# Kernel optimization log

Hardware: AMD Instinct MI355X
Metric: run time of the kernel (lower is better)

## Reference

```python
import jax, jax.numpy as jnp
import numpy as np
from jax import lax

B, C_IN, J, T = 32, 3, 64, 256
C_OUT = 64
S_LEN = 5           # spatial_length
T_LEN = 7           # temporal_length
T_PAD = (T_LEN - 1) // 2
EPS = 1e-5
SIG_IN = C_IN + 1   # +1 time channel from signatory.Augment(include_time=True)
SIG_CH = SIG_IN + SIG_IN**2 + SIG_IN**3  # signature_channels(depth=3) = 84


def sig3(pts):
    """Depth-3 path signature with basepoint=True. pts: [N, L, c] -> [N, c + c^2 + c^3]."""
    N, L, c = pts.shape
    # basepoint=True prepends the origin, so first increment is pts[:, 0]
    incs = jnp.concatenate([pts[:, :1], jnp.diff(pts, axis=1)], axis=1)  # [N, L, c]
    S1 = jnp.zeros((N, c), pts.dtype)
    S2 = jnp.zeros((N, c, c), pts.dtype)
    S3 = jnp.zeros((N, c, c, c), pts.dtype)

    def step(carry, d):  # Chen's identity: S <- S tensor exp(d)
        S1, S2, S3 = carry
        e2 = 0.5 * d[:, :, None] * d[:, None, :]               # d^2/2
        S3 = (S3
              + S2[:, :, :, None] * d[:, None, None, :]
              + S1[:, :, None, None] * e2[:, None, :, :]
              + d[:, :, None, None] * e2[:, None, :, :] / 3.0)  # d^3/6
        S2 = S2 + S1[:, :, None] * d[:, None, :] + e2
        S1 = S1 + d
        return (S1, S2, S3), None

    (S1, S2, S3), _ = lax.scan(step, (S1, S2, S3), jnp.swapaxes(incs, 0, 1))
    return jnp.concatenate([S1, S2.reshape(N, c * c), S3.reshape(N, c * c * c)], axis=1)


def signet(pts, W, b):
    """SigNet: time-augment, depth-3 signature, linear. pts: [N, L, C_IN]."""
    N, L, _ = pts.shape
    t = jnp.linspace(0.0, 1.0, L, dtype=pts.dtype)
    aug = jnp.concatenate([pts, jnp.broadcast_to(t[None, :, None], (N, L, 1))], axis=2)
    return sig3(aug) @ W.T + b


def bn(x, g, be, m, v):  # eval-mode BatchNorm2d, x [B,C,H,W]
    scale = (g / jnp.sqrt(v + EPS))[None, :, None, None]
    return (x - m[None, :, None, None]) * scale + be[None, :, None, None]


def setup_inputs() -> dict:
    key = jax.random.key(0)
    ks = jax.random.split(key, 12)
    d = {}
    d['x'] = jax.random.normal(ks[0], (B, C_IN, J, T), jnp.float32)
    d['path'] = jax.random.randint(ks[1], (J, S_LEN), 0, J, jnp.int32)
    d['W_ssig'] = jax.random.normal(ks[2], (C_OUT, SIG_CH), jnp.float32) * 0.05
    d['b_ssig'] = jnp.zeros((C_OUT,), jnp.float32)
    d['W_tsig'] = jax.random.normal(ks[3], (C_OUT, SIG_CH), jnp.float32) * 0.05
    d['b_tsig'] = jnp.zeros((C_OUT,), jnp.float32)
    d['W_raw'] = jax.random.normal(ks[4], (C_OUT, C_IN, 1, 3), jnp.float32) * 0.1
    d['b_raw'] = jnp.zeros((C_OUT,), jnp.float32)
    d['W_ps'] = jax.random.normal(ks[5], (C_OUT, 2 * C_OUT), jnp.float32) * 0.05
    d['b_ps'] = jnp.zeros((C_OUT,), jnp.float32)
    d['W_fu'] = jax.random.normal(ks[6], (C_OUT, 2 * C_OUT), jnp.float32) * 0.05
    d['b_fu'] = jnp.zeros((C_OUT,), jnp.float32)
    for tag in ('raw', 'ps', 'fu'):
        d['g_' + tag] = jnp.ones((C_OUT,), jnp.float32)
        d['be_' + tag] = jnp.zeros((C_OUT,), jnp.float32)
        d['m_' + tag] = jnp.zeros((C_OUT,), jnp.float32)
        d['v_' + tag] = jnp.ones((C_OUT,), jnp.float32)
    return d


def reference(x, path, W_ssig, b_ssig, W_tsig, b_tsig, W_raw, b_raw, W_ps, b_ps,
              W_fu, b_fu, g_raw, be_raw, m_raw, v_raw, g_ps, be_ps, m_ps, v_ps,
              g_fu, be_fu, m_fu, v_fu):
    Bx, C, Jx, Tx = x.shape
    # raw branch: Conv2d (1,3) pad (0,1) + BN + ReLU
    x_conv = lax.conv_general_dilated(x, W_raw, (1, 1), ((0, 0), (1, 1)),
                                      dimension_numbers=('NCHW', 'OIHW', 'NCHW'))
    x_conv = jax.nn.relu(bn(x_conv + b_raw[None, :, None, None], g_raw, be_raw, m_raw, v_raw))

    # spatial branch: gather joint paths -> [B*T*J, S_LEN, C]
    g = x[:, :, path, :]                                      # [B, C, J, S, T]
    sp = jnp.transpose(g, (0, 4, 2, 3, 1)).reshape(Bx * Tx * Jx, S_LEN, C)
    ss = signet(sp, W_ssig, b_ssig).reshape(Bx, Tx, Jx, C_OUT)
    ss = jnp.transpose(ss, (0, 3, 2, 1))                      # [B, C_OUT, J, T]

    # temporal branch: replicate-pad + unfold windows
    xp = jnp.pad(x, ((0, 0), (0, 0), (0, 0), (T_PAD, T_PAD)), mode='edge')
    tw = jnp.stack([xp[..., k:k + Tx] for k in range(T_LEN)], axis=2)  # [B, C, T_LEN, J, T]
    tw = tw.reshape(Bx, C, Jx, T_LEN, Tx)                     # faithful torch reshape (reinterprets memory)
    tp = jnp.transpose(tw, (0, 4, 2, 3, 1)).reshape(Bx * Tx * Jx, T_LEN, C)
    ts = signet(tp, W_tsig, b_tsig).reshape(Bx, Tx, Jx, C_OUT)
    ts = jnp.transpose(ts, (0, 3, 2, 1))                      # [B, C_OUT, J, T]

    # ps_fusion: 1x1 conv + BN + ReLU over concat(spatial, temporal)
    sig = jnp.concatenate([ss, ts], axis=1)                   # [B, 2*C_OUT, J, T]
    sig = jnp.einsum('oc,bcjt->bojt', W_ps, sig) + b_ps[None, :, None, None]
    sig = jax.nn.relu(bn(sig, g_ps, be_ps, m_ps, v_ps))

    # final fusion
    x_out = jnp.concatenate([x_conv, sig], axis=1)            # [B, 2*C_OUT, J, T]
    x_out = jnp.einsum('oc,bcjt->bojt', W_fu, x_out) + b_fu[None, :, None, None]
    x_out = jax.nn.relu(bn(x_out, g_fu, be_fu, m_fu, v_fu))
    return x_out
```

## Files before the change

### kernel.cpp

```cpp
#include <hip/hip_runtime.h>
#include <cstdint>

#define EPSF 1e-5f

typedef __attribute__((ext_vector_type(8))) short     bf16x8;
typedef __attribute__((ext_vector_type(4))) float     f32x4;
typedef __attribute__((ext_vector_type(4))) unsigned int uint32x4;
typedef __attribute__((ext_vector_type(2))) unsigned int uint32x2;

#define WS_B0 0
#define WS_BC 64
#define WS_BF 128

__device__ __forceinline__ unsigned short f2bf(float f) {
    union { float f; unsigned u; } v; v.f = f;
    unsigned r = v.u + 0x7fffu + ((v.u >> 16) & 1u);
    return (unsigned short)(r >> 16);
}

__device__ __forceinline__ unsigned cvtpk(float lo, float hi) {
    unsigned r;
    asm("v_cvt_pk_bf16_f32 %0, %1, %2" : "=v"(r) : "v"(lo), "v"(hi));
    return r;
}

__global__ __launch_bounds__(64) void stem_prep(
    const float* __restrict__ W_ssig, const float* __restrict__ b_ssig,
    const float* __restrict__ W_tsig, const float* __restrict__ b_tsig,
    const float* __restrict__ W_raw,  const float* __restrict__ b_raw,
    const float* __restrict__ W_ps,   const float* __restrict__ b_ps,
    const float* __restrict__ W_fu,   const float* __restrict__ b_fu,
    const float* __restrict__ g_raw, const float* __restrict__ be_raw,
    const float* __restrict__ m_raw, const float* __restrict__ v_raw,
    const float* __restrict__ g_ps,  const float* __restrict__ be_ps,
    const float* __restrict__ m_ps,  const float* __restrict__ v_ps,
    const float* __restrict__ g_fu,  const float* __restrict__ be_fu,
    const float* __restrict__ m_fu,  const float* __restrict__ v_fu,
    float* __restrict__ wsf, unsigned short* __restrict__ wsA1,
    unsigned short* __restrict__ wsA2, unsigned short* __restrict__ wsA3)
{
    const int l = threadIdx.x;
    const int f = blockIdx.x;
    if (f < 24) {
        const int h = f / 12, rem = f % 12, s = rem / 4, to = rem % 4;
        const int o = to*16 + (l & 15);
        const float sps = g_ps[o] / sqrtf(v_ps[o] + EPSF);
        const float* wp  = W_ps + o*128 + 64*h;
        const float* wsg = h ? W_tsig : W_ssig;
        for (int b = 0; b < 8; ++b) {
            const int k = s*32 + ((l >> 4) * 8) + b;
            float v = 0.f;
            if (k < 84) {
                float acc = 0.f;
                for (int c = 0; c < 64; ++c) acc = fmaf(wp[c], wsg[c*84 + k], acc);
                v = acc * sps;
            }
            wsA1[f*512 + l*8 + b] = f2bf(v);
        }
    } else if (f < 40) {
        const int q = f - 24, s = q / 4, to = q % 4;
        const int o = to*16 + (l & 15);
        const float sfu = g_fu[o] / sqrtf(v_fu[o] + EPSF);
        for (int b = 0; b < 8; ++b) {
            const int c = s*32 + ((l >> 4) * 8) + b;
            wsA2[q*512 + l*8 + b] = f2bf(W_fu[o*128 + c] * sfu);
        }
    } else if (f == 40) {
        const int o = l;
        const float sps = g_ps[o] / sqrtf(v_ps[o] + EPSF);
        float acc = b_ps[o] - m_ps[o];
        for (int c = 0; c < 64; ++c) {
            acc = fmaf(W_ps[o*128 + c],      b_ssig[c], acc);
            acc = fmaf(W_ps[o*128 + 64 + c], b_tsig[c], acc);
        }
        wsf[WS_B0 + o] = acc * sps + be_ps[o];
        const float sraw = g_raw[o] / sqrtf(v_raw[o] + EPSF);
        wsf[WS_BC + o] = (b_raw[o] - m_raw[o]) * sraw + be_raw[o];
        const float sfu = g_fu[o] / sqrtf(v_fu[o] + EPSF);
        wsf[WS_BF + o] = (b_fu[o] - m_fu[o]) * sfu + be_fu[o];
    } else {
        const int to = f - 41;
        const int o = to*16 + (l & 15);
        const float sraw = g_raw[o] / sqrtf(v_raw[o] + EPSF);
        for (int b = 0; b < 8; ++b) {
            const int k = ((l >> 4) * 8) + b;
            wsA3[to*512 + l*8 + b] = (k < 9) ? f2bf(W_raw[o*9 + k] * sraw) : (unsigned short)0;
        }
    }
}

__device__ __forceinline__ void sig_step(float* __restrict__ sig, const float d[4])
{
    float* S1 = sig; float* S2 = sig + 4; float* S3 = sig + 20;
    float dh[4], fv[4];
#pragma unroll
    for (int i = 0; i < 4; ++i) dh[i] = 0.5f * d[i];
#pragma unroll
    for (int i = 0; i < 4; ++i) fv[i] = fmaf(d[i], (1.f/3.f), S1[i]);
    float h[16];
#pragma unroll
    for (int i = 0; i < 4; ++i)
#pragma unroll
        for (int j = 0; j < 4; ++j) h[i*4+j] = fmaf(fv[i], dh[j], S2[i*4+j]);
#pragma unroll
    for (int i = 0; i < 4; ++i)
#pragma unroll
        for (int j = 0; j < 4; ++j) {
            const float hij = h[i*4+j];
#pragma unroll
            for (int k = 0; k < 4; ++k)
                S3[(i*4+j)*4+k] = fmaf(hij, d[k], S3[(i*4+j)*4+k]);
        }
    float q[4];
#pragma unroll
    for (int i = 0; i < 4; ++i) q[i] = S1[i] + dh[i];
#pragma unroll
    for (int i = 0; i < 4; ++i)
#pragma unroll
        for (int j = 0; j < 4; ++j) S2[i*4+j] = fmaf(q[i], d[j], S2[i*4+j]);
#pragma unroll
    for (int i = 0; i < 4; ++i) S1[i] += d[i];
}

__device__ __forceinline__ void sig_init(float* __restrict__ sig, float d0, float d1, float d2)
{
    const float dd[4] = { d0, d1, d2, 0.f };
#pragma unroll
    for (int i = 0; i < 4; ++i) sig[i] = dd[i];
#pragma unroll
    for (int i = 0; i < 4; ++i) {
        const float dh = 0.5f * dd[i];
#pragma unroll
        for (int j = 0; j < 4; ++j) sig[4 + i*4 + j] = dh * dd[j];
    }
#pragma unroll
    for (int i = 0; i < 4; ++i) {
        const float di3 = dd[i] * (1.f/3.f);
#pragma unroll
        for (int j = 0; j < 4; ++j)
#pragma unroll
            for (int k = 0; k < 4; ++k)
                sig[20 + (i*4+j)*4 + k] = di3 * sig[4 + j*4 + k];
    }
}

__global__ __launch_bounds__(64, 3) void stem_main(
    const float* __restrict__ x, const int* __restrict__ path,
    const float* __restrict__ wsf, const unsigned short* __restrict__ wsA1,
    const unsigned short* __restrict__ wsA2, const unsigned short* __restrict__ wsA3,
    float* __restrict__ out)
{
    __shared__ char sb[12 * 1024];
    const int l  = threadIdx.x;
    const int t  = blockIdx.x * 64 + l;
    const int j  = blockIdx.y;
    const int b  = blockIdx.z;
    const float* xb = x + (size_t)b * (3*64*256);

    const int lg = l >> 4;
    const int li = l & 15;
    char* const myw = sb + l*16;

    float ps_[5][3];
#pragma unroll
    for (int s = 0; s < 5; ++s) {
        const int jp = path[j*5 + s];
        ps_[s][0] = xb[(0*64 + jp)*256 + t];
        ps_[s][1] = xb[(1*64 + jp)*256 + t];
        ps_[s][2] = xb[(2*64 + jp)*256 + t];
    }
    float pt_[7][3];
#pragma unroll
    for (int k = 0; k < 7; ++k) {
        const int idx  = j*7 + k;
        const int jsrc = idx & 63;
        const int tl   = idx >> 6;
        const int ts   = min(max(t + tl - 3, 0), 255);
        pt_[k][0] = xb[(0*64 + jsrc)*256 + ts];
        pt_[k][1] = xb[(1*64 + jsrc)*256 + ts];
        pt_[k][2] = xb[(2*64 + jsrc)*256 + ts];
    }

    float sig[84];
    {
        sig_init(sig, ps_[0][0], ps_[0][1], ps_[0][2]);
#pragma unroll
        for (int s = 1; s < 5; ++s) {
            const float d[4] = { ps_[s][0]-ps_[s-1][0], ps_[s][1]-ps_[s-1][1],
                                 ps_[s][2]-ps_[s-1][2], 0.25f };
            sig_step(sig, d);
        }
    }
    {
        unsigned uu[48];
#pragma unroll
        for (int i = 0; i < 42; ++i) uu[i] = cvtpk(sig[2*i], sig[2*i+1]);
#pragma unroll
        for (int i = 42; i < 48; ++i) uu[i] = 0u;
#pragma unroll
        for (int v = 0; v < 12; ++v) {
            uint32x4 w = { uu[4*v], uu[4*v+1], uu[4*v+2], uu[4*v+3] };
            *(uint32x4*)(myw + v*1024) = w;
        }
    }
    __syncthreads();

    unsigned uuT[48];
    {
        sig_init(sig, pt_[0][0], pt_[0][1], pt_[0][2]);
#pragma unroll
        for (int k = 1; k < 7; ++k) {
            const float d[4] = { pt_[k][0]-pt_[k-1][0], pt_[k][1]-pt_[k-1][1],
                                 pt_[k][2]-pt_[k-1][2], (1.f/6.f) };
            sig_step(sig, d);
        }
#pragma unroll
        for (int i = 0; i < 42; ++i) uuT[i] = cvtpk(sig[2*i], sig[2*i+1]);
#pragma unroll
        for (int i = 42; i < 48; ++i) uuT[i] = 0u;
    }

    f32x4 acc[4][4];
#pragma unroll
    for (int to = 0; to < 4; ++to) {
        const f32x4 b0 = *(const f32x4*)(wsf + WS_B0 + to*16 + lg*4);
#pragma unroll
        for (int tt = 0; tt < 4; ++tt) acc[to][tt] = b0;
    }
    {
#pragma unroll
        for (int s = 0; s < 3; ++s) {
            bf16x8 A0 = *(const bf16x8*)(wsA1 + ((0*3+s)*4+0)*512 + l*8);
            bf16x8 A1 = *(const bf16x8*)(wsA1 + ((0*3+s)*4+1)*512 + l*8);
            bf16x8 A2 = *(const bf16x8*)(wsA1 + ((0*3+s)*4+2)*512 + l*8);
            bf16x8 A3 = *(const bf16x8*)(wsA1 + ((0*3+s)*4+3)*512 + l*8);
#pragma unroll
            for (int tt = 0; tt < 4; ++tt) {
                const bf16x8 B = *(const bf16x8*)(sb + (s*4+lg)*1024 + (tt*16+li)*16);
                acc[0][tt] = __builtin_amdgcn_mfma_f32_16x16x32_bf16(A0, B, acc[0][tt], 0, 0, 0);
                acc[1][tt] = __builtin_amdgcn_mfma_f32_16x16x32_bf16(A1, B, acc[1][tt], 0, 0, 0);
                acc[2][tt] = __builtin_amdgcn_mfma_f32_16x16x32_bf16(A2, B, acc[2][tt], 0, 0, 0);
                acc[3][tt] = __builtin_amdgcn_mfma_f32_16x16x32_bf16(A3, B, acc[3][tt], 0, 0, 0);
            }
        }
    }
    __syncthreads();

    {
#pragma unroll
        for (int v = 0; v < 12; ++v) {
            uint32x4 w = { uuT[4*v], uuT[4*v+1], uuT[4*v+2], uuT[4*v+3] };
            *(uint32x4*)(myw + v*1024) = w;
        }
    }
    __syncthreads();

    float xv[9];
#pragma unroll
    for (int ci = 0; ci < 3; ++ci) {
        const float* xr = xb + (ci*64 + j)*256;
        xv[ci*3+0] = (t >= 1)   ? xr[t-1] : 0.f;
        xv[ci*3+1] = xr[t];
        xv[ci*3+2] = (t <= 254) ? xr[t+1] : 0.f;
    }

    {
#pragma unroll
        for (int s = 0; s < 3; ++s) {
            bf16x8 A0 = *(const bf16x8*)(wsA1 + ((1*3+s)*4+0)*512 + l*8);
            bf16x8 A1 = *(const bf16x8*)(wsA1 + ((1*3+s)*4+1)*512 + l*8);
            bf16x8 A2 = *(const bf16x8*)(wsA1 + ((1*3+s)*4+2)*512 + l*8);
            bf16x8 A3 = *(const bf16x8*)(wsA1 + ((1*3+s)*4+3)*512 + l*8);
#pragma unroll
            for (int tt = 0; tt < 4; ++tt) {
                const bf16x8 B = *(const bf16x8*)(sb + (s*4+lg)*1024 + (tt*16+li)*16);
                acc[0][tt] = __builtin_amdgcn_mfma_f32_16x16x32_bf16(A0, B, acc[0][tt], 0, 0, 0);
                acc[1][tt] = __builtin_amdgcn_mfma_f32_16x16x32_bf16(A1, B, acc[1][tt], 0, 0, 0);
                acc[2][tt] = __builtin_amdgcn_mfma_f32_16x16x32_bf16(A2, B, acc[2][tt], 0, 0, 0);
                acc[3][tt] = __builtin_amdgcn_mfma_f32_16x16x32_bf16(A3, B, acc[3][tt], 0, 0, 0);
            }
        }
    }
    __syncthreads();

#pragma unroll
    for (int to = 0; to < 4; ++to) {
#pragma unroll
        for (int tt = 0; tt < 4; ++tt) {
            const unsigned w0 = cvtpk(fmaxf(acc[to][tt][0], 0.f), fmaxf(acc[to][tt][1], 0.f));
            const unsigned w1 = cvtpk(fmaxf(acc[to][tt][2], 0.f), fmaxf(acc[to][tt][3], 0.f));
            uint32x2 w = { w0, w1 };
            *(uint32x2*)(sb + (to*2+(lg>>1))*1024 + (tt*16+li)*16 + ((lg&1)<<3)) = w;
        }
    }
    {
        unsigned xu[16];
        xu[0] = cvtpk(xv[0], xv[1]); xu[1] = cvtpk(xv[2], xv[3]);
        xu[2] = cvtpk(xv[4], xv[5]); xu[3] = cvtpk(xv[6], xv[7]);
        xu[4] = cvtpk(xv[8], 0.f);
#pragma unroll
        for (int i = 5; i < 16; ++i) xu[i] = 0u;
#pragma unroll
        for (int v = 0; v < 4; ++v) {
            uint32x4 w = { xu[4*v], xu[4*v+1], xu[4*v+2], xu[4*v+3] };
            *(uint32x4*)(myw + (8+v)*1024) = w;
        }
    }
    __syncthreads();

#pragma unroll
    for (int to = 0; to < 4; ++to) {
        const f32x4 bc4 = *(const f32x4*)(wsf + WS_BC + to*16 + lg*4);
#pragma unroll
        for (int tt = 0; tt < 4; ++tt) acc[to][tt] = bc4;
    }
    {
        bf16x8 A0 = *(const bf16x8*)(wsA3 + 0*512 + l*8);
        bf16x8 A1 = *(const bf16x8*)(wsA3 + 1*512 + l*8);
        bf16x8 A2 = *(const bf16x8*)(wsA3 + 2*512 + l*8);
        bf16x8 A3 = *(const bf16x8*)(wsA3 + 3*512 + l*8);
#pragma unroll
        for (int tt = 0; tt < 4; ++tt) {
            const bf16x8 B = *(const bf16x8*)(sb + (8+lg)*1024 + (tt*16+li)*16);
            acc[0][tt] = __builtin_amdgcn_mfma_f32_16x16x32_bf16(A0, B, acc[0][tt], 0, 0, 0);
            acc[1][tt] = __builtin_amdgcn_mfma_f32_16x16x32_bf16(A1, B, acc[1][tt], 0, 0, 0);
            acc[2][tt] = __builtin_amdgcn_mfma_f32_16x16x32_bf16(A2, B, acc[2][tt], 0, 0, 0);
            acc[3][tt] = __builtin_amdgcn_mfma_f32_16x16x32_bf16(A3, B, acc[3][tt], 0, 0, 0);
        }
    }
    unsigned cu[32];
#pragma unroll
    for (int to = 0; to < 4; ++to)
#pragma unroll
        for (int tt = 0; tt < 4; ++tt) {
            cu[(to*4+tt)*2+0] = cvtpk(fmaxf(acc[to][tt][0], 0.f), fmaxf(acc[to][tt][1], 0.f));
            cu[(to*4+tt)*2+1] = cvtpk(fmaxf(acc[to][tt][2], 0.f), fmaxf(acc[to][tt][3], 0.f));
        }

#pragma unroll
    for (int to = 0; to < 4; ++to) {
        const f32x4 bf4 = *(const f32x4*)(wsf + WS_BF + to*16 + lg*4);
#pragma unroll
        for (int tt = 0; tt < 4; ++tt) acc[to][tt] = bf4;
    }
    {
#pragma unroll
        for (int s = 0; s < 2; ++s) {
            bf16x8 A0 = *(const bf16x8*)(wsA2 + ((s+2)*4+0)*512 + l*8);
            bf16x8 A1 = *(const bf16x8*)(wsA2 + ((s+2)*4+1)*512 + l*8);
            bf16x8 A2 = *(const bf16x8*)(wsA2 + ((s+2)*4+2)*512 + l*8);
            bf16x8 A3 = *(const bf16x8*)(wsA2 + ((s+2)*4+3)*512 + l*8);
#pragma unroll
            for (int tt = 0; tt < 4; ++tt) {
                const bf16x8 B = *(const bf16x8*)(sb + (s*4+lg)*1024 + (tt*16+li)*16);
                acc[0][tt] = __builtin_amdgcn_mfma_f32_16x16x32_bf16(A0, B, acc[0][tt], 0, 0, 0);
                acc[1][tt] = __builtin_amdgcn_mfma_f32_16x16x32_bf16(A1, B, acc[1][tt], 0, 0, 0);
                acc[2][tt] = __builtin_amdgcn_mfma_f32_16x16x32_bf16(A2, B, acc[2][tt], 0, 0, 0);
                acc[3][tt] = __builtin_amdgcn_mfma_f32_16x16x32_bf16(A3, B, acc[3][tt], 0, 0, 0);
            }
        }
    }
    __syncthreads();

#pragma unroll
    for (int to = 0; to < 4; ++to)
#pragma unroll
        for (int tt = 0; tt < 4; ++tt) {
            uint32x2 w = { cu[(to*4+tt)*2+0], cu[(to*4+tt)*2+1] };
            *(uint32x2*)(sb + (to*2+(lg>>1))*1024 + (tt*16+li)*16 + ((lg&1)<<3)) = w;
        }
    __syncthreads();

    {
#pragma unroll
        for (int s = 0; s < 2; ++s) {
            bf16x8 A0 = *(const bf16x8*)(wsA2 + (s*4+0)*512 + l*8);
            bf16x8 A1 = *(const bf16x8*)(wsA2 + (s*4+1)*512 + l*8);
            bf16x8 A2 = *(const bf16x8*)(wsA2 + (s*4+2)*512 + l*8);
            bf16x8 A3 = *(const bf16x8*)(wsA2 + (s*4+3)*512 + l*8);
#pragma unroll
            for (int tt = 0; tt < 4; ++tt) {
                const bf16x8 B = *(const bf16x8*)(sb + (s*4+lg)*1024 + (tt*16+li)*16);
                acc[0][tt] = __builtin_amdgcn_mfma_f32_16x16x32_bf16(A0, B, acc[0][tt], 0, 0, 0);
                acc[1][tt] = __builtin_amdgcn_mfma_f32_16x16x32_bf16(A1, B, acc[1][tt], 0, 0, 0);
                acc[2][tt] = __builtin_amdgcn_mfma_f32_16x16x32_bf16(A2, B, acc[2][tt], 0, 0, 0);
                acc[3][tt] = __builtin_amdgcn_mfma_f32_16x16x32_bf16(A3, B, acc[3][tt], 0, 0, 0);
            }
        }
    }

#pragma unroll
    for (int to = 0; to < 4; ++to) {
#pragma unroll
        for (int tt = 0; tt < 4; ++tt) {
            const int tg = blockIdx.x*64 + tt*16 + li;
#pragma unroll
            for (int r = 0; r < 4; ++r) {
                const int o = to*16 + lg*4 + r;
                out[(((size_t)b*64 + o)*64 + j)*256 + tg] = fmaxf(acc[to][tt][r], 0.f);
            }
        }
    }
}

extern "C" void kernel_launch(void* const* d_in, const int* in_sizes, int n_in,
                              void* d_out, int out_size, void* d_ws, size_t ws_size,
                              hipStream_t stream)
{
    const float* x      = (const float*)d_in[0];
    const int*   path   = (const int*)  d_in[1];
    const float* W_ssig = (const float*)d_in[2];
    const float* b_ssig = (const float*)d_in[3];
    const float* W_tsig = (const float*)d_in[4];
    const float* b_tsig = (const float*)d_in[5];
    const float* W_raw  = (const float*)d_in[6];
    const float* b_raw  = (const float*)d_in[7];
    const float* W_ps   = (const float*)d_in[8];
    const float* b_ps   = (const float*)d_in[9];
    const float* W_fu   = (const float*)d_in[10];
    const float* b_fu   = (const float*)d_in[11];
    const float* g_raw  = (const float*)d_in[12];
    const float* be_raw = (const float*)d_in[13];
    const float* m_raw  = (const float*)d_in[14];
    const float* v_raw  = (const float*)d_in[15];
    const float* g_ps   = (const float*)d_in[16];
    const float* be_ps  = (const float*)d_in[17];
    const float* m_ps   = (const float*)d_in[18];
    const float* v_ps   = (const float*)d_in[19];
    const float* g_fu   = (const float*)d_in[20];
    const float* be_fu  = (const float*)d_in[21];
    const float* m_fu   = (const float*)d_in[22];
    const float* v_fu   = (const float*)d_in[23];
    float* out = (float*)d_out;

    float*          wsf  = (float*)d_ws;
    unsigned short* wsA1 = (unsigned short*)((char*)d_ws + 4096);
    unsigned short* wsA2 = (unsigned short*)((char*)d_ws + 28672);
    unsigned short* wsA3 = (unsigned short*)((char*)d_ws + 45056);

    stem_prep<<<45, 64, 0, stream>>>(W_ssig, b_ssig, W_tsig, b_tsig, W_raw, b_raw,
                                     W_ps, b_ps, W_fu, b_fu,
                                     g_raw, be_raw, m_raw, v_raw,
                                     g_ps, be_ps, m_ps, v_ps,
                                     g_fu, be_fu, m_fu, v_fu, wsf, wsA1, wsA2, wsA3);

    dim3 grid(4, 64, 32);
    stem_main<<<grid, 64, 0, stream>>>(x, path, wsf, wsA1, wsA2, wsA3, out);
}
```

Measured before the change: 64.08 us.

## Compute path signatures in packed fp16 and switch MFMA to fp16

Replaces the fp32 scalar signature recurrence with packed-half arithmetic (v_pk_fma_f16 and op_sel broadcasts), so each instruction updates two signature terms and the state fits in 42 registers instead of 84. All MFMA operands and weights move from bf16 to fp16 to match, which removes the separate fp32-to-bf16 packing step. This roughly halves the VALU work and register pressure of the signature stage. The trade-off is reduced precision and range: the signature is accumulated in fp16 and conversions use round-toward-zero, which could overflow or lose accuracy on large inputs.

Result: faster. 60.57 us (-5.5%).

```diff
diff --git a/kernel.cpp b/kernel.cpp
--- a/kernel.cpp
+++ b/kernel.cpp
@@ -1,9 +1,10 @@
 #include <hip/hip_runtime.h>
+#include <hip/hip_fp16.h>
 #include <cstdint>
 
 #define EPSF 1e-5f
 
-typedef __attribute__((ext_vector_type(8))) short     bf16x8;
+typedef __attribute__((ext_vector_type(8))) _Float16  f16x8;
 typedef __attribute__((ext_vector_type(4))) float     f32x4;
 typedef __attribute__((ext_vector_type(4))) unsigned int uint32x4;
 typedef __attribute__((ext_vector_type(2))) unsigned int uint32x2;
@@ -12,17 +13,41 @@
 #define WS_BC 64
 #define WS_BF 128
 
-__device__ __forceinline__ unsigned short f2bf(float f) {
-    union { float f; unsigned u; } v; v.f = f;
-    unsigned r = v.u + 0x7fffu + ((v.u >> 16) & 1u);
-    return (unsigned short)(r >> 16);
-}
-
-__device__ __forceinline__ unsigned cvtpk(float lo, float hi) {
+__device__ __forceinline__ unsigned short f2h(float f) {
+    __half h = __float2half(f);
+    return *reinterpret_cast<unsigned short*>(&h);
+}
+
+__device__ __forceinline__ unsigned cvtpk_h(float lo, float hi) {
     unsigned r;
-    asm("v_cvt_pk_bf16_f32 %0, %1, %2" : "=v"(r) : "v"(lo), "v"(hi));
+    asm("v_cvt_pkrtz_f16_f32 %0, %1, %2" : "=v"(r) : "v"(lo), "v"(hi));
     return r;
 }
+
+__device__ __forceinline__ unsigned pkfma(unsigned a, unsigned b, unsigned c) {
+    unsigned d; asm("v_pk_fma_f16 %0, %1, %2, %3" : "=v"(d) : "v"(a), "v"(b), "v"(c)); return d;
+}
+__device__ __forceinline__ unsigned pkfma_lo(unsigned a, unsigned b, unsigned c) {
+    unsigned d; asm("v_pk_fma_f16 %0, %1, %2, %3 op_sel_hi:[0,1,1]" : "=v"(d) : "v"(a), "v"(b), "v"(c)); return d;
+}
+__device__ __forceinline__ unsigned pkfma_hi(unsigned a, unsigned b, unsigned c) {
+    unsigned d; asm("v_pk_fma_f16 %0, %1, %2, %3 op_sel:[1,0,0]" : "=v"(d) : "v"(a), "v"(b), "v"(c)); return d;
+}
+__device__ __forceinline__ unsigned pkmul(unsigned a, unsigned b) {
+    unsigned d; asm("v_pk_mul_f16 %0, %1, %2" : "=v"(d) : "v"(a), "v"(b)); return d;
+}
+__device__ __forceinline__ unsigned pkmul_lo(unsigned a, unsigned b) {
+    unsigned d; asm("v_pk_mul_f16 %0, %1, %2 op_sel_hi:[0,1]" : "=v"(d) : "v"(a), "v"(b)); return d;
+}
+__device__ __forceinline__ unsigned pkmul_hi(unsigned a, unsigned b) {
+    unsigned d; asm("v_pk_mul_f16 %0, %1, %2 op_sel:[1,0]" : "=v"(d) : "v"(a), "v"(b)); return d;
+}
+__device__ __forceinline__ unsigned pkadd(unsigned a, unsigned b) {
+    unsigned d; asm("v_pk_add_f16 %0, %1, %2" : "=v"(d) : "v"(a), "v"(b)); return d;
+}
+
+#define C_HALF2  0x38003800u
+#define C_THIRD2 0x35553555u
 
 __global__ __launch_bounds__(64) void stem_prep(
     const float* __restrict__ W_ssig, const float* __restrict__ b_ssig,
@@ -55,7 +80,7 @@
                 for (int c = 0; c < 64; ++c) acc = fmaf(wp[c], wsg[c*84 + k], acc);
                 v = acc * sps;
             }
-            wsA1[f*512 + l*8 + b] = f2bf(v);
+            wsA1[f*512 + l*8 + b] = f2h(v);
         }
     } else if (f < 40) {
         const int q = f - 24, s = q / 4, to = q % 4;
@@ -63,7 +88,7 @@
         const float sfu = g_fu[o] / sqrtf(v_fu[o] + EPSF);
         for (int b = 0; b < 8; ++b) {
             const int c = s*32 + ((l >> 4) * 8) + b;
-            wsA2[q*512 + l*8 + b] = f2bf(W_fu[o*128 + c] * sfu);
+            wsA2[q*512 + l*8 + b] = f2h(W_fu[o*128 + c] * sfu);
         }
     } else if (f == 40) {
         const int o = l;
@@ -84,63 +109,61 @@
         const float sraw = g_raw[o] / sqrtf(v_raw[o] + EPSF);
         for (int b = 0; b < 8; ++b) {
             const int k = ((l >> 4) * 8) + b;
-            wsA3[to*512 + l*8 + b] = (k < 9) ? f2bf(W_raw[o*9 + k] * sraw) : (unsigned short)0;
-        }
-    }
-}
-
-__device__ __forceinline__ void sig_step(float* __restrict__ sig, const float d[4])
+            wsA3[to*512 + l*8 + b] = (k < 9) ? f2h(W_raw[o*9 + k] * sraw) : (unsigned short)0;
+        }
+    }
+}
+
+__device__ __forceinline__ void sig_step_h(unsigned* __restrict__ S, unsigned d01, unsigned d23)
 {
-    float* S1 = sig; float* S2 = sig + 4; float* S3 = sig + 20;
-    float dh[4], fv[4];
-#pragma unroll
-    for (int i = 0; i < 4; ++i) dh[i] = 0.5f * d[i];
-#pragma unroll
-    for (int i = 0; i < 4; ++i) fv[i] = fmaf(d[i], (1.f/3.f), S1[i]);
-    float h[16];
-#pragma unroll
-    for (int i = 0; i < 4; ++i)
-#pragma unroll
-        for (int j = 0; j < 4; ++j) h[i*4+j] = fmaf(fv[i], dh[j], S2[i*4+j]);
-#pragma unroll
-    for (int i = 0; i < 4; ++i)
+    const unsigned dh0 = pkmul(C_HALF2, d01), dh1 = pkmul(C_HALF2, d23);
+    const unsigned fv0 = pkfma(d01, C_THIRD2, S[0]);
+    const unsigned fv1 = pkfma(d23, C_THIRD2, S[1]);
+    unsigned h[8];
+    h[0] = pkfma_lo(fv0, dh0, S[2]); h[1] = pkfma_lo(fv0, dh1, S[3]);
+    h[2] = pkfma_hi(fv0, dh0, S[4]); h[3] = pkfma_hi(fv0, dh1, S[5]);
+    h[4] = pkfma_lo(fv1, dh0, S[6]); h[5] = pkfma_lo(fv1, dh1, S[7]);
+    h[6] = pkfma_hi(fv1, dh0, S[8]); h[7] = pkfma_hi(fv1, dh1, S[9]);
+#pragma unroll
+    for (int i = 0; i < 4; ++i) {
 #pragma unroll
         for (int j = 0; j < 4; ++j) {
-            const float hij = h[i*4+j];
-#pragma unroll
-            for (int k = 0; k < 4; ++k)
-                S3[(i*4+j)*4+k] = fmaf(hij, d[k], S3[(i*4+j)*4+k]);
-        }
-    float q[4];
-#pragma unroll
-    for (int i = 0; i < 4; ++i) q[i] = S1[i] + dh[i];
-#pragma unroll
-    for (int i = 0; i < 4; ++i)
-#pragma unroll
-        for (int j = 0; j < 4; ++j) S2[i*4+j] = fmaf(q[i], d[j], S2[i*4+j]);
-#pragma unroll
-    for (int i = 0; i < 4; ++i) S1[i] += d[i];
-}
-
-__device__ __forceinline__ void sig_init(float* __restrict__ sig, float d0, float d1, float d2)
+            const int hr = i*2 + (j>>1);
+            const int base = 10 + (i*4+j)*2;
+            if (j & 1) { S[base]   = pkfma_hi(h[hr], d01, S[base]);
+                         S[base+1] = pkfma_hi(h[hr], d23, S[base+1]); }
+            else       { S[base]   = pkfma_lo(h[hr], d01, S[base]);
+                         S[base+1] = pkfma_lo(h[hr], d23, S[base+1]); }
+        }
+    }
+    const unsigned q0 = pkadd(S[0], dh0), q1 = pkadd(S[1], dh1);
+    S[2] = pkfma_lo(q0, d01, S[2]); S[3] = pkfma_lo(q0, d23, S[3]);
+    S[4] = pkfma_hi(q0, d01, S[4]); S[5] = pkfma_hi(q0, d23, S[5]);
+    S[6] = pkfma_lo(q1, d01, S[6]); S[7] = pkfma_lo(q1, d23, S[7]);
+    S[8] = pkfma_hi(q1, d01, S[8]); S[9] = pkfma_hi(q1, d23, S[9]);
+    S[0] = pkadd(S[0], d01); S[1] = pkadd(S[1], d23);
+}
+
+__device__ __forceinline__ void sig_init_h(unsigned* __restrict__ S, unsigned d01, unsigned d23)
 {
-    const float dd[4] = { d0, d1, d2, 0.f };
-#pragma unroll
-    for (int i = 0; i < 4; ++i) sig[i] = dd[i];
+    S[0] = d01; S[1] = d23;
+    const unsigned dh0 = pkmul(C_HALF2, d01), dh1 = pkmul(C_HALF2, d23);
+    S[2] = pkmul_lo(dh0, d01); S[3] = pkmul_lo(dh0, d23);
+    S[4] = pkmul_hi(dh0, d01); S[5] = pkmul_hi(dh0, d23);
+    S[6] = pkmul_lo(dh1, d01); S[7] = pkmul_lo(dh1, d23);
+    S[8] = pkmul_hi(dh1, d01); S[9] = pkmul_hi(dh1, d23);
+    const unsigned td0 = pkmul(C_THIRD2, d01), td1 = pkmul(C_THIRD2, d23);
 #pragma unroll
     for (int i = 0; i < 4; ++i) {
-        const float dh = 0.5f * dd[i];
-#pragma unroll
-        for (int j = 0; j < 4; ++j) sig[4 + i*4 + j] = dh * dd[j];
-    }
-#pragma unroll
-    for (int i = 0; i < 4; ++i) {
-        const float di3 = dd[i] * (1.f/3.f);
-#pragma unroll
-        for (int j = 0; j < 4; ++j)
-#pragma unroll
-            for (int k = 0; k < 4; ++k)
-                sig[20 + (i*4+j)*4 + k] = di3 * sig[4 + j*4 + k];
+        const unsigned tdr = (i < 2) ? td0 : td1;
+#pragma unroll
+        for (int j = 0; j < 4; ++j) {
+            const int base = 10 + (i*4+j)*2;
+            if (i & 1) { S[base]   = pkmul_hi(tdr, S[2+j*2]);
+                         S[base+1] = pkmul_hi(tdr, S[2+j*2+1]); }
+            else       { S[base]   = pkmul_lo(tdr, S[2+j*2]);
+                         S[base+1] = pkmul_lo(tdr, S[2+j*2+1]); }
+        }
     }
 }
 
@@ -181,43 +204,32 @@
         pt_[k][2] = xb[(2*64 + jsrc)*256 + ts];
     }
 
-    float sig[84];
-    {
-        sig_init(sig, ps_[0][0], ps_[0][1], ps_[0][2]);
-#pragma unroll
-        for (int s = 1; s < 5; ++s) {
-            const float d[4] = { ps_[s][0]-ps_[s-1][0], ps_[s][1]-ps_[s-1][1],
-                                 ps_[s][2]-ps_[s-1][2], 0.25f };
-            sig_step(sig, d);
-        }
-    }
-    {
-        unsigned uu[48];
-#pragma unroll
-        for (int i = 0; i < 42; ++i) uu[i] = cvtpk(sig[2*i], sig[2*i+1]);
-#pragma unroll
-        for (int i = 42; i < 48; ++i) uu[i] = 0u;
-#pragma unroll
-        for (int v = 0; v < 12; ++v) {
-            uint32x4 w = { uu[4*v], uu[4*v+1], uu[4*v+2], uu[4*v+3] };
+    unsigned S[42];
+
+    sig_init_h(S, cvtpk_h(ps_[0][0], ps_[0][1]), cvtpk_h(ps_[0][2], 0.f));
+#pragma unroll
+    for (int s = 1; s < 5; ++s) {
+        const unsigned d01 = cvtpk_h(ps_[s][0]-ps_[s-1][0], ps_[s][1]-ps_[s-1][1]);
+        const unsigned d23 = cvtpk_h(ps_[s][2]-ps_[s-1][2], 0.25f);
+        sig_step_h(S, d01, d23);
+    }
+    {
+#pragma unroll
+        for (int v = 0; v < 10; ++v) {
+            uint32x4 w = { S[4*v], S[4*v+1], S[4*v+2], S[4*v+3] };
             *(uint32x4*)(myw + v*1024) = w;
         }
-    }
-    __syncthreads();
-
-    unsigned uuT[48];
-    {
-        sig_init(sig, pt_[0][0], pt_[0][1], pt_[0][2]);
-#pragma unroll
-        for (int k = 1; k < 7; ++k) {
-            const float d[4] = { pt_[k][0]-pt_[k-1][0], pt_[k][1]-pt_[k-1][1],
-                                 pt_[k][2]-pt_[k-1][2], (1.f/6.f) };
-            sig_step(sig, d);
-        }
-#pragma unroll
-        for (int i = 0; i < 42; ++i) uuT[i] = cvtpk(sig[2*i], sig[2*i+1]);
-#pragma unroll
-        for (int i = 42; i < 48; ++i) uuT[i] = 0u;
+        uint32x4 w10 = { S[40], S[41], 0u, 0u }; *(uint32x4*)(myw + 10*1024) = w10;
+        uint32x4 w11 = { 0u, 0u, 0u, 0u };       *(uint32x4*)(myw + 11*1024) = w11;
+    }
+    __syncthreads();
+
+    sig_init_h(S, cvtpk_h(pt_[0][0], pt_[0][1]), cvtpk_h(pt_[0][2], 0.f));
+#pragma unroll
+    for (int k = 1; k < 7; ++k) {
+        const unsigned d01 = cvtpk_h(pt_[k][0]-pt_[k-1][0], pt_[k][1]-pt_[k-1][1]);
+        const unsigned d23 = cvtpk_h(pt_[k][2]-pt_[k-1][2], (1.f/6.f));
+        sig_step_h(S, d01, d23);
     }
 
     f32x4 acc[4][4];
@@ -230,28 +242,29 @@
     {
 #pragma unroll
         for (int s = 0; s < 3; ++s) {
-            bf16x8 A0 = *(const bf16x8*)(wsA1 + ((0*3+s)*4+0)*512 + l*8);
-            bf16x8 A1 = *(const bf16x8*)(wsA1 + ((0*3+s)*4+1)*512 + l*8);
-            bf16x8 A2 = *(const bf16x8*)(wsA1 + ((0*3+s)*4+2)*512 + l*8);
-            bf16x8 A3 = *(const bf16x8*)(wsA1 + ((0*3+s)*4+3)*512 + l*8);
+            f16x8 A0 = *(const f16x8*)(wsA1 + ((0*3+s)*4+0)*512 + l*8);
+            f16x8 A1 = *(const f16x8*)(wsA1 + ((0*3+s)*4+1)*512 + l*8);
+            f16x8 A2 = *(const f16x8*)(wsA1 + ((0*3+s)*4+2)*512 + l*8);
+            f16x8 A3 = *(const f16x8*)(wsA1 + ((0*3+s)*4+3)*512 + l*8);
 #pragma unroll
             for (int tt = 0; tt < 4; ++tt) {
-                const bf16x8 B = *(const bf16x8*)(sb + (s*4+lg)*1024 + (tt*16+li)*16);
-                acc[0][tt] = __builtin_amdgcn_mfma_f32_16x16x32_bf16(A0, B, acc[0][tt], 0, 0, 0);
-                acc[1][tt] = __builtin_amdgcn_mfma_f32_16x16x32_bf16(A1, B, acc[1][tt], 0, 0, 0);
-                acc[2][tt] = __builtin_amdgcn_mfma_f32_16x16x32_bf16(A2, B, acc[2][tt], 0, 0, 0);
-                acc[3][tt] = __builtin_amdgcn_mfma_f32_16x16x32_bf16(A3, B, acc[3][tt], 0, 0, 0);
-            }
-        }
-    }
-    __syncthreads();
-
-    {
-#pragma unroll
-        for (int v = 0; v < 12; ++v) {
-            uint32x4 w = { uuT[4*v], uuT[4*v+1], uuT[4*v+2], uuT[4*v+3] };
+                const f16x8 B = *(const f16x8*)(sb + (s*4+lg)*1024 + (tt*16+li)*16);
+                acc[0][tt] = __builtin_amdgcn_mfma_f32_16x16x32_f16(A0, B, acc[0][tt], 0, 0, 0);
+                acc[1][tt] = __builtin_amdgcn_mfma_f32_16x16x32_f16(A1, B, acc[1][tt], 0, 0, 0);
+                acc[2][tt] = __builtin_amdgcn_mfma_f32_16x16x32_f16(A2, B, acc[2][tt], 0, 0, 0);
+                acc[3][tt] = __builtin_amdgcn_mfma_f32_16x16x32_f16(A3, B, acc[3][tt], 0, 0, 0);
+            }
+        }
+    }
+    __syncthreads();
+
+    {
+#pragma unroll
+        for (int v = 0; v < 10; ++v) {
+            uint32x4 w = { S[4*v], S[4*v+1], S[4*v+2], S[4*v+3] };
             *(uint32x4*)(myw + v*1024) = w;
         }
+        uint32x4 w10 = { S[40], S[41], 0u, 0u }; *(uint32x4*)(myw + 10*1024) = w10;
     }
     __syncthreads();
 
@@ -267,17 +280,17 @@
     {
 #pragma unroll
         for (int s = 0; s < 3; ++s) {
-            bf16x8 A0 = *(const bf16x8*)(wsA1 + ((1*3+s)*4+0)*512 + l*8);
-            bf16x8 A1 = *(const bf16x8*)(wsA1 + ((1*3+s)*4+1)*512 + l*8);
-            bf16x8 A2 = *(const bf16x8*)(wsA1 + ((1*3+s)*4+2)*512 + l*8);
-            bf16x8 A3 = *(const bf16x8*)(wsA1 + ((1*3+s)*4+3)*512 + l*8);
+            f16x8 A0 = *(const f16x8*)(wsA1 + ((1*3+s)*4+0)*512 + l*8);
+            f16x8 A1 = *(const f16x8*)(wsA1 + ((1*3+s)*4+1)*512 + l*8);
+            f16x8 A2 = *(const f16x8*)(wsA1 + ((1*3+s)*4+2)*512 + l*8);
+            f16x8 A3 = *(const f16x8*)(wsA1 + ((1*3+s)*4+3)*512 + l*8);
 #pragma unroll
             for (int tt = 0; tt < 4; ++tt) {
-                const bf16x8 B = *(const bf16x8*)(sb + (s*4+lg)*1024 + (tt*16+li)*16);
-                acc[0][tt] = __builtin_amdgcn_mfma_f32_16x16x32_bf16(A0, B, acc[0][tt], 0, 0, 0);
-                acc[1][tt] = __builtin_amdgcn_mfma_f32_16x16x32_bf16(A1, B, acc[1][tt], 0, 0, 0);
-                acc[2][tt] = __builtin_amdgcn_mfma_f32_16x16x32_bf16(A2, B, acc[2][tt], 0, 0, 0);
-                acc[3][tt] = __builtin_amdgcn_mfma_f32_16x16x32_bf16(A3, B, acc[3][tt], 0, 0, 0);
+                const f16x8 B = *(const f16x8*)(sb + (s*4+lg)*1024 + (tt*16+li)*16);
+                acc[0][tt] = __builtin_amdgcn_mfma_f32_16x16x32_f16(A0, B, acc[0][tt], 0, 0, 0);
+                acc[1][tt] = __builtin_amdgcn_mfma_f32_16x16x32_f16(A1, B, acc[1][tt], 0, 0, 0);
+                acc[2][tt] = __builtin_amdgcn_mfma_f32_16x16x32_f16(A2, B, acc[2][tt], 0, 0, 0);
+                acc[3][tt] = __builtin_amdgcn_mfma_f32_16x16x32_f16(A3, B, acc[3][tt], 0, 0, 0);
             }
         }
     }
@@ -287,17 +300,17 @@
     for (int to = 0; to < 4; ++to) {
 #pragma unroll
         for (int tt = 0; tt < 4; ++tt) {
-            const unsigned w0 = cvtpk(fmaxf(acc[to][tt][0], 0.f), fmaxf(acc[to][tt][1], 0.f));
-            const unsigned w1 = cvtpk(fmaxf(acc[to][tt][2], 0.f), fmaxf(acc[to][tt][3], 0.f));
+            const unsigned w0 = cvtpk_h(fmaxf(acc[to][tt][0], 0.f), fmaxf(acc[to][tt][1], 0.f));
+            const unsigned w1 = cvtpk_h(fmaxf(acc[to][tt][2], 0.f), fmaxf(acc[to][tt][3], 0.f));
             uint32x2 w = { w0, w1 };
             *(uint32x2*)(sb + (to*2+(lg>>1))*1024 + (tt*16+li)*16 + ((lg&1)<<3)) = w;
         }
     }
     {
         unsigned xu[16];
-        xu[0] = cvtpk(xv[0], xv[1]); xu[1] = cvtpk(xv[2], xv[3]);
-        xu[2] = cvtpk(xv[4], xv[5]); xu[3] = cvtpk(xv[6], xv[7]);
-        xu[4] = cvtpk(xv[8], 0.f);
+        xu[0] = cvtpk_h(xv[0], xv[1]); xu[1] = cvtpk_h(xv[2], xv[3]);
+        xu[2] = cvtpk_h(xv[4], xv[5]); xu[3] = cvtpk_h(xv[6], xv[7]);
+        xu[4] = cvtpk_h(xv[8], 0.f);
 #pragma unroll
         for (int i = 5; i < 16; ++i) xu[i] = 0u;
 #pragma unroll
@@ -315,17 +328,17 @@
         for (int tt = 0; tt < 4; ++tt) acc[to][tt] = bc4;
     }
     {
-        bf16x8 A0 = *(const bf16x8*)(wsA3 + 0*512 + l*8);
-        bf16x8 A1 = *(const bf16x8*)(wsA3 + 1*512 + l*8);
-        bf16x8 A2 = *(const bf16x8*)(wsA3 + 2*512 + l*8);
-        bf16x8 A3 = *(const bf16x8*)(wsA3 + 3*512 + l*8);
+        f16x8 A0 = *(const f16x8*)(wsA3 + 0*512 + l*8);
+        f16x8 A1 = *(const f16x8*)(wsA3 + 1*512 + l*8);
+        f16x8 A2 = *(const f16x8*)(wsA3 + 2*512 + l*8);
+        f16x8 A3 = *(const f16x8*)(wsA3 + 3*512 + l*8);
 #pragma unroll
         for (int tt = 0; tt < 4; ++tt) {
-            const bf16x8 B = *(const bf16x8*)(sb + (8+lg)*1024 + (tt*16+li)*16);
-            acc[0][tt] = __builtin_amdgcn_mfma_f32_16x16x32_bf16(A0, B, acc[0][tt], 0, 0, 0);
-            acc[1][tt] = __builtin_amdgcn_mfma_f32_16x16x32_bf16(A1, B, acc[1][tt], 0, 0, 0);
-            acc[2][tt] = __builtin_amdgcn_mfma_f32_16x16x32_bf16(A2, B, acc[2][tt], 0, 0, 0);
-            acc[3][tt] = __builtin_amdgcn_mfma_f32_16x16x32_bf16(A3, B, acc[3][tt], 0, 0, 0);
+            const f16x8 B = *(const f16x8*)(sb + (8+lg)*1024 + (tt*16+li)*16);
+            acc[0][tt] = __builtin_amdgcn_mfma_f32_16x16x32_f16(A0, B, acc[0][tt], 0, 0, 0);
+            acc[1][tt] = __builtin_amdgcn_mfma_f32_16x16x32_f16(A1, B, acc[1][tt], 0, 0, 0);
+            acc[2][tt] = __builtin_amdgcn_mfma_f32_16x16x32_f16(A2, B, acc[2][tt], 0, 0, 0);
+            acc[3][tt] = __builtin_amdgcn_mfma_f32_16x16x32_f16(A3, B, acc[3][tt], 0, 0, 0);
         }
     }
     unsigned cu[32];
@@ -333,8 +346,8 @@
     for (int to = 0; to < 4; ++to)
 #pragma unroll
         for (int tt = 0; tt < 4; ++tt) {
-            cu[(to*4+tt)*2+0] = cvtpk(fmaxf(acc[to][tt][0], 0.f), fmaxf(acc[to][tt][1], 0.f));
-            cu[(to*4+tt)*2+1] = cvtpk(fmaxf(acc[to][tt][2], 0.f), fmaxf(acc[to][tt][3], 0.f));
+            cu[(to*4+tt)*2+0] = cvtpk_h(fmaxf(acc[to][tt][0], 0.f), fmaxf(acc[to][tt][1], 0.f));
+            cu[(to*4+tt)*2+1] = cvtpk_h(fmaxf(acc[to][tt][2], 0.f), fmaxf(acc[to][tt][3], 0.f));
         }
 
 #pragma unroll
@@ -346,17 +359,17 @@
     {
 #pragma unroll
         for (int s = 0; s < 2; ++s) {
-            bf16x8 A0 = *(const bf16x8*)(wsA2 + ((s+2)*4+0)*512 + l*8);
-            bf16x8 A1 = *(const bf16x8*)(wsA2 + ((s+2)*4+1)*512 + l*8);
-            bf16x8 A2 = *(const bf16x8*)(wsA2 + ((s+2)*4+2)*512 + l*8);
-            bf16x8 A3 = *(const bf16x8*)(wsA2 + ((s+2)*4+3)*512 + l*8);
+            f16x8 A0 = *(const f16x8*)(wsA2 + ((s+2)*4+0)*512 + l*8);
+            f16x8 A1 = *(const f16x8*)(wsA2 + ((s+2)*4+1)*512 + l*8);
+            f16x8 A2 = *(const f16x8*)(wsA2 + ((s+2)*4+2)*512 + l*8);
+            f16x8 A3 = *(const f16x8*)(wsA2 + ((s+2)*4+3)*512 + l*8);
 #pragma unroll
             for (int tt = 0; tt < 4; ++tt) {
-                const bf16x8 B = *(const bf16x8*)(sb + (s*4+lg)*1024 + (tt*16+li)*16);
-                acc[0][tt] = __builtin_amdgcn_mfma_f32_16x16x32_bf16(A0, B, acc[0][tt], 0, 0, 0);
-                acc[1][tt] = __builtin_amdgcn_mfma_f32_16x16x32_bf16(A1, B, acc[1][tt], 0, 0, 0);
-                acc[2][tt] = __builtin_amdgcn_mfma_f32_16x16x32_bf16(A2, B, acc[2][tt], 0, 0, 0);
-                acc[3][tt] = __builtin_amdgcn_mfma_f32_16x16x32_bf16(A3, B, acc[3][tt], 0, 0, 0);
+                const f16x8 B = *(const f16x8*)(sb + (s*4+lg)*1024 + (tt*16+li)*16);
+                acc[0][tt] = __builtin_amdgcn_mfma_f32_16x16x32_f16(A0, B, acc[0][tt], 0, 0, 0);
+                acc[1][tt] = __builtin_amdgcn_mfma_f32_16x16x32_f16(A1, B, acc[1][tt], 0, 0, 0);
+                acc[2][tt] = __builtin_amdgcn_mfma_f32_16x16x32_f16(A2, B, acc[2][tt], 0, 0, 0);
+                acc[3][tt] = __builtin_amdgcn_mfma_f32_16x16x32_f16(A3, B, acc[3][tt], 0, 0, 0);
             }
         }
     }
@@ -374,17 +387,17 @@
     {
 #pragma unroll
         for (int s = 0; s < 2; ++s) {
-            bf16x8 A0 = *(const bf16x8*)(wsA2 + (s*4+0)*512 + l*8);
-            bf16x8 A1 = *(const bf16x8*)(wsA2 + (s*4+1)*512 + l*8);
-            bf16x8 A2 = *(const bf16x8*)(wsA2 + (s*4+2)*512 + l*8);
-            bf16x8 A3 = *(const bf16x8*)(wsA2 + (s*4+3)*512 + l*8);
+            f16x8 A0 = *(const f16x8*)(wsA2 + (s*4+0)*512 + l*8);
+            f16x8 A1 = *(const f16x8*)(wsA2 + (s*4+1)*512 + l*8);
+            f16x8 A2 = *(const f16x8*)(wsA2 + (s*4+2)*512 + l*8);
+            f16x8 A3 = *(const f16x8*)(wsA2 + (s*4+3)*512 + l*8);
 #pragma unroll
             for (int tt = 0; tt < 4; ++tt) {
-                const bf16x8 B = *(const bf16x8*)(sb + (s*4+lg)*1024 + (tt*16+li)*16);
-                acc[0][tt] = __builtin_amdgcn_mfma_f32_16x16x32_bf16(A0, B, acc[0][tt], 0, 0, 0);
-                acc[1][tt] = __builtin_amdgcn_mfma_f32_16x16x32_bf16(A1, B, acc[1][tt], 0, 0, 0);
-                acc[2][tt] = __builtin_amdgcn_mfma_f32_16x16x32_bf16(A2, B, acc[2][tt], 0, 0, 0);
-                acc[3][tt] = __builtin_amdgcn_mfma_f32_16x16x32_bf16(A3, B, acc[3][tt], 0, 0, 0);
+                const f16x8 B = *(const f16x8*)(sb + (s*4+lg)*1024 + (tt*16+li)*16);
+                acc[0][tt] = __builtin_amdgcn_mfma_f32_16x16x32_f16(A0, B, acc[0][tt], 0, 0, 0);
+                acc[1][tt] = __builtin_amdgcn_mfma_f32_16x16x32_f16(A1, B, acc[1][tt], 0, 0, 0);
+                acc[2][tt] = __builtin_amdgcn_mfma_f32_16x16x32_f16(A2, B, acc[2][tt], 0, 0, 0);
+                acc[3][tt] = __builtin_amdgcn_mfma_f32_16x16x32_f16(A3, B, acc[3][tt], 0, 0, 0);
             }
         }
     }
```
